# Kernel tuning notes

Measured on AMD Instinct MI355X. Metric: run time of the kernel, lower is better.

Reference implementation:

```python
import jax, jax.numpy as jnp
import numpy as np

IN_CH, OUT_CH, K, DIL, COND = 16, 16, 3, 4, 8
B, T_OUT = 32, 65536
PAD = DIL * (K - 1)


def setup_inputs() -> dict:
    key = jax.random.key(0)
    ks = jax.random.split(key, 6)
    return {
        "x": jax.random.normal(ks[0], (B, IN_CH, T_OUT + PAD), dtype=jnp.float32),
        "p": jax.random.normal(ks[1], (B, COND), dtype=jnp.float32),
        "W1": jax.random.normal(ks[2], (COND, IN_CH), dtype=jnp.float32) * 0.3,
        "b1": jax.random.normal(ks[3], (IN_CH,), dtype=jnp.float32) * 0.1,
        "W2": jax.random.normal(ks[4], (IN_CH, IN_CH * OUT_CH * K), dtype=jnp.float32) * 0.1,
        "b2": jax.random.normal(ks[5], (IN_CH * OUT_CH * K,), dtype=jnp.float32) * 0.05,
    }


def reference(x, p, W1, b1, W2, b2):
    # hypernetwork: per-sample conv weights from condition vector p
    h = p @ W1 + b1                      # [B, in_ch]
    h = jnp.where(h > 0, h, 0.2 * h)     # LeakyReLU(0.2)
    w = (h @ W2 + b2).reshape(B, IN_CH * K, OUT_CH)  # [B, in_ch*K, out_ch]

    # im2col-style gather of K dilated shifted slices, concatenated on channel dim
    start, end = PAD, x.shape[-1]
    x_cat = jnp.concatenate(
        [x[:, :, start - i * DIL : end - i * DIL] for i in range(K)], axis=1
    )  # [B, in_ch*K, T_out]

    # batched GEMM: [B, T, in_ch*K] x [B, in_ch*K, out_ch] -> output [B, out_ch, T]
    y = jnp.einsum("bct,bco->bot", x_cat, w)
    return y
```

## Files before the change

### kernel.cpp

```cpp
#include <hip/hip_runtime.h>


#define NB 32
#define IN_CH 16
#define OUT_CH 16
#define KW 3
#define DIL 4
#define COND 8
#define T_OUT 65536
#define PADT 8
#define XT (T_OUT + PADT)
#define W2COLS (IN_CH * OUT_CH * KW)
#define TPB 256
#define TPT 4
#define T_PER_BLOCK (TPB * TPT)
#define BLOCKS_PER_B (T_OUT / T_PER_BLOCK)
#define ROWF (T_PER_BLOCK + PADT)
#define NBUF 4

typedef const __attribute__((address_space(1))) void* gvp;
typedef __attribute__((address_space(3))) void* svp;
typedef float f32x4 __attribute__((ext_vector_type(4)));

__device__ __forceinline__ void stage_row(const float* __restrict__ g,
                                          float* l, int wid, int lane)
{
    __builtin_amdgcn_global_load_lds((gvp)(g + wid * 256 + lane * 4),
                                     (svp)(l + wid * 256), 16, 0, 0);
    if (wid == 0 && lane < 2)
        __builtin_amdgcn_global_load_lds((gvp)(g + 1024 + lane * 4),
                                         (svp)(l + 1024), 16, 0, 0);
}

__device__ __forceinline__ void compute_row(const float* __restrict__ xrow,
                                            const float* __restrict__ w_lds,
                                            int c, float4* acc, int tid)
{
    const float4 l0 = *(const float4*)(xrow + tid * 4);
    const float4 l1 = *(const float4*)(xrow + tid * 4 + 4);
    const float4 l2 = *(const float4*)(xrow + tid * 4 + 8);
    const float4 vs[KW] = {l2, l1, l0};
#pragma unroll
    for (int i = 0; i < KW; ++i) {
        const float4 v = vs[i];
        const float* wrow = w_lds + (i * IN_CH + c) * OUT_CH;
#pragma unroll
        for (int og = 0; og < 4; ++og) {
            const float4 wv = *(const float4*)(wrow + og * 4);
            float4* a = acc + og * 4;
            a[0].x += v.x * wv.x; a[0].y += v.y * wv.x;
            a[0].z += v.z * wv.x; a[0].w += v.w * wv.x;
            a[1].x += v.x * wv.y; a[1].y += v.y * wv.y;
            a[1].z += v.z * wv.y; a[1].w += v.w * wv.y;
            a[2].x += v.x * wv.z; a[2].y += v.y * wv.z;
            a[2].z += v.z * wv.z; a[2].w += v.w * wv.z;
            a[3].x += v.x * wv.w; a[3].y += v.y * wv.w;
            a[3].z += v.z * wv.w; a[3].w += v.w * wv.w;
        }
    }
}

__global__ __launch_bounds__(TPB)
void hyperconv_kernel(const float* __restrict__ x,
                      const float* __restrict__ p,
                      const float* __restrict__ W1,
                      const float* __restrict__ b1,
                      const float* __restrict__ W2,
                      const float* __restrict__ b2,
                      float* __restrict__ y)
{
    __shared__ __align__(16) float xbuf[NBUF][ROWF];
    __shared__ float h_lds[IN_CH];
    __shared__ __align__(16) float w_lds[W2COLS];

    const int tid    = threadIdx.x;
    const int wid    = tid >> 6;
    const int lane   = tid & 63;
    const int b      = blockIdx.x / BLOCKS_PER_B;
    const int tchunk = blockIdx.x % BLOCKS_PER_B;
    const int t0b    = tchunk * T_PER_BLOCK;

    const float* xrb = x + (size_t)b * IN_CH * XT + t0b;

    stage_row(xrb + 0 * XT, xbuf[0], wid, lane);
    stage_row(xrb + 1 * XT, xbuf[1], wid, lane);
    stage_row(xrb + 2 * XT, xbuf[2], wid, lane);

    if (tid < IN_CH) {
        float acc = b1[tid];
#pragma unroll
        for (int j = 0; j < COND; ++j)
            acc += p[b * COND + j] * W1[j * IN_CH + tid];
        h_lds[tid] = acc > 0.f ? acc : 0.2f * acc;
    }
    __syncthreads();

#pragma unroll
    for (int r = 0; r < 3; ++r) {
        const int n = tid * 3 + r;
        float acc = b2[n];
#pragma unroll
        for (int c = 0; c < IN_CH; ++c)
            acc += h_lds[c] * W2[c * W2COLS + n];
        w_lds[n] = acc;
    }
    __syncthreads();

    float4 acc[OUT_CH];
#pragma unroll
    for (int o = 0; o < OUT_CH; ++o) acc[o] = make_float4(0.f, 0.f, 0.f, 0.f);

    for (int c = 0; c < 13; ++c) {
        __builtin_amdgcn_sched_barrier(0);
        stage_row(xrb + (c + 3) * XT, xbuf[(c + 3) & 3], wid, lane);
        if (wid == 0) asm volatile("s_waitcnt vmcnt(6)" ::: "memory");
        else          asm volatile("s_waitcnt vmcnt(3)" ::: "memory");
        __builtin_amdgcn_s_barrier();
        __builtin_amdgcn_sched_barrier(0);
        compute_row(xbuf[c & 3], w_lds, c, acc, tid);
        __builtin_amdgcn_sched_barrier(0);
        __builtin_amdgcn_s_barrier();
    }
    asm volatile("s_waitcnt vmcnt(0)" ::: "memory");
    __builtin_amdgcn_s_barrier();
    __builtin_amdgcn_sched_barrier(0);
    compute_row(xbuf[13 & 3], w_lds, 13, acc, tid);
    compute_row(xbuf[14 & 3], w_lds, 14, acc, tid);
    compute_row(xbuf[15 & 3], w_lds, 15, acc, tid);

    float* yb = y + (size_t)b * OUT_CH * T_OUT + t0b + tid * TPT;
#pragma unroll
    for (int o = 0; o < OUT_CH; ++o) {
        const float4 a = acc[o];
        f32x4 v = {a.x, a.y, a.z, a.w};
        __builtin_nontemporal_store(v, (f32x4*)(yb + o * T_OUT));
    }
}

extern "C" void kernel_launch(void* const* d_in, const int* in_sizes, int n_in,
                              void* d_out, int out_size, void* d_ws, size_t ws_size,
                              hipStream_t stream) {
    const float* x  = (const float*)d_in[0];
    const float* p  = (const float*)d_in[1];
    const float* W1 = (const float*)d_in[2];
    const float* b1 = (const float*)d_in[3];
    const float* W2 = (const float*)d_in[4];
    const float* b2 = (const float*)d_in[5];
    float* y = (float*)d_out;

    dim3 grid(NB * BLOCKS_PER_B);
    dim3 block(TPB);
    hyperconv_kernel<<<grid, block, 0, stream>>>(x, p, W1, b1, W2, b2, y);
}
```

Before: 246.1 us.

## Make blocks persistent over multiple tiles with continuous cross-tile prefetch pipeline

```diff
diff --git a/kernel.cpp b/kernel.cpp
--- a/kernel.cpp
+++ b/kernel.cpp
@@ -5,7 +5,6 @@
 #define IN_CH 16
 #define OUT_CH 16
 #define KW 3
-#define DIL 4
 #define COND 8
 #define T_OUT 65536
 #define PADT 8
@@ -13,10 +12,14 @@
 #define W2COLS (IN_CH * OUT_CH * KW)
 #define TPB 256
 #define TPT 4
-#define T_PER_BLOCK (TPB * TPT)
-#define BLOCKS_PER_B (T_OUT / T_PER_BLOCK)
-#define ROWF (T_PER_BLOCK + PADT)
+#define T_PER_TILE (TPB * TPT)
+#define TILES_PER_B (T_OUT / T_PER_TILE)
+#define GROUPS 16
+#define TILES_PER_BLOCK (TILES_PER_B / GROUPS)
+#define NR (TILES_PER_BLOCK * IN_CH)
+#define ROWF (T_PER_TILE + PADT)
 #define NBUF 4
+#define GRID (NB * GROUPS)
 
 typedef const __attribute__((address_space(1))) void* gvp;
 typedef __attribute__((address_space(3))) void* svp;
@@ -28,8 +31,8 @@
     __builtin_amdgcn_global_load_lds((gvp)(g + wid * 256 + lane * 4),
                                      (svp)(l + wid * 256), 16, 0, 0);
     if (wid == 0 && lane < 2)
-        __builtin_amdgcn_global_load_lds((gvp)(g + 1024 + lane * 4),
-                                         (svp)(l + 1024), 16, 0, 0);
+        __builtin_amdgcn_global_load_lds((gvp)(g + T_PER_TILE + lane * 4),
+                                         (svp)(l + T_PER_TILE), 16, 0, 0);
 }
 
 __device__ __forceinline__ void compute_row(const float* __restrict__ xrow,
@@ -73,18 +76,20 @@
     __shared__ float h_lds[IN_CH];
     __shared__ __align__(16) float w_lds[W2COLS];
 
-    const int tid    = threadIdx.x;
-    const int wid    = tid >> 6;
-    const int lane   = tid & 63;
-    const int b      = blockIdx.x / BLOCKS_PER_B;
-    const int tchunk = blockIdx.x % BLOCKS_PER_B;
-    const int t0b    = tchunk * T_PER_BLOCK;
+    const int tid   = threadIdx.x;
+    const int wid   = tid >> 6;
+    const int lane  = tid & 63;
+    const int b     = blockIdx.x >> 4;
+    const int group = blockIdx.x & 15;
 
-    const float* xrb = x + (size_t)b * IN_CH * XT + t0b;
+    const float* xb_base = x + (size_t)b * IN_CH * XT;
 
-    stage_row(xrb + 0 * XT, xbuf[0], wid, lane);
-    stage_row(xrb + 1 * XT, xbuf[1], wid, lane);
-    stage_row(xrb + 2 * XT, xbuf[2], wid, lane);
+#define ROW_PTR(r) (xb_base + (size_t)((r) & 15) * XT \
+                    + (group + GROUPS * ((r) >> 4)) * T_PER_TILE)
+
+    stage_row(ROW_PTR(0), xbuf[0], wid, lane);
+    stage_row(ROW_PTR(1), xbuf[1], wid, lane);
+    stage_row(ROW_PTR(2), xbuf[2], wid, lane);
 
     if (tid < IN_CH) {
         float acc = b1[tid];
@@ -110,31 +115,38 @@
 #pragma unroll
     for (int o = 0; o < OUT_CH; ++o) acc[o] = make_float4(0.f, 0.f, 0.f, 0.f);
 
-    for (int c = 0; c < 13; ++c) {
+#pragma unroll 1
+    for (int r = 0; r < NR; ++r) {
         __builtin_amdgcn_sched_barrier(0);
-        stage_row(xrb + (c + 3) * XT, xbuf[(c + 3) & 3], wid, lane);
-        if (wid == 0) asm volatile("s_waitcnt vmcnt(6)" ::: "memory");
-        else          asm volatile("s_waitcnt vmcnt(3)" ::: "memory");
+        if (r + 3 < NR)
+            stage_row(ROW_PTR(r + 3), xbuf[(r + 3) & 3], wid, lane);
+        if (r >= NR - 3) {
+            asm volatile("s_waitcnt vmcnt(0)" ::: "memory");
+        } else if ((r & 15) < 3 && r >= 16) {
+            if (wid == 0) asm volatile("s_waitcnt vmcnt(22)" ::: "memory");
+            else          asm volatile("s_waitcnt vmcnt(19)" ::: "memory");
+        } else {
+            if (wid == 0) asm volatile("s_waitcnt vmcnt(6)" ::: "memory");
+            else          asm volatile("s_waitcnt vmcnt(3)" ::: "memory");
+        }
         __builtin_amdgcn_s_barrier();
         __builtin_amdgcn_sched_barrier(0);
-        compute_row(xbuf[c & 3], w_lds, c, acc, tid);
+        compute_row(xbuf[r & 3], w_lds, r & 15, acc, tid);
         __builtin_amdgcn_sched_barrier(0);
+        if ((r & 15) == 15) {
+            float* yb = y + (size_t)b * OUT_CH * T_OUT
+                      + (group + GROUPS * (r >> 4)) * T_PER_TILE + tid * TPT;
+#pragma unroll
+            for (int o = 0; o < OUT_CH; ++o) {
+                const float4 a = acc[o];
+                f32x4 v = {a.x, a.y, a.z, a.w};
+                __builtin_nontemporal_store(v, (f32x4*)(yb + o * T_OUT));
+                acc[o] = make_float4(0.f, 0.f, 0.f, 0.f);
+            }
+        }
         __builtin_amdgcn_s_barrier();
     }
-    asm volatile("s_waitcnt vmcnt(0)" ::: "memory");
-    __builtin_amdgcn_s_barrier();
-    __builtin_amdgcn_sched_barrier(0);
-    compute_row(xbuf[13 & 3], w_lds, 13, acc, tid);
-    compute_row(xbuf[14 & 3], w_lds, 14, acc, tid);
-    compute_row(xbuf[15 & 3], w_lds, 15, acc, tid);
-
-    float* yb = y + (size_t)b * OUT_CH * T_OUT + t0b + tid * TPT;
-#pragma unroll
-    for (int o = 0; o < OUT_CH; ++o) {
-        const float4 a = acc[o];
-        f32x4 v = {a.x, a.y, a.z, a.w};
-        __builtin_nontemporal_store(v, (f32x4*)(yb + o * T_OUT));
-    }
+#undef ROW_PTR
 }
 
 extern "C" void kernel_launch(void* const* d_in, const int* in_sizes, int n_in,
@@ -148,7 +160,7 @@
     const float* b2 = (const float*)d_in[5];
     float* y = (float*)d_out;
 
-    dim3 grid(NB * BLOCKS_PER_B);
+    dim3 grid(GRID);
     dim3 block(TPB);
     hyperconv_kernel<<<grid, block, 0, stream>>>(x, p, W1, b1, W2, b2, y);
 }
```

New measurement: 269.5 us. 1.1x slower.
